# Kernel tuning notes

Hardware: AMD Instinct MI355X
Metric: run time of the kernel (lower is better)

Reference implementation:

```python
import jax, jax.numpy as jnp
import numpy as np

N_NODES = 100000
N_EDGES = 1600000
N_GRAPHS = 1024
DIM_IN = 128
DIM_SF = 32
DIM_OUT = 8
EPS = 1e-5


def setup_inputs() -> dict:
    key = jax.random.key(0)
    ks = jax.random.split(key, 16)
    feat = jax.random.normal(ks[0], (N_NODES, DIM_IN), dtype=jnp.float32)
    self_feat = jax.random.normal(ks[1], (N_GRAPHS, DIM_SF), dtype=jnp.float32)
    src = jax.random.randint(ks[2], (N_EDGES,), 0, N_NODES)
    dst = jax.random.randint(ks[3], (N_EDGES,), 0, N_NODES)
    node2graph = jnp.sort(jax.random.randint(ks[4], (N_NODES,), 0, N_GRAPHS))

    def lin(k, din, dout):
        s = 1.0 / np.sqrt(din)
        kw, kb = jax.random.split(k)
        W = jax.random.uniform(kw, (din, dout), minval=-s, maxval=s, dtype=jnp.float32)
        b = jax.random.uniform(kb, (dout,), minval=-s, maxval=s, dtype=jnp.float32)
        return W, b

    W1, b1 = lin(ks[5], DIM_IN, 100)
    W2, b2 = lin(ks[6], 100, 20)
    Wf1, bf1 = lin(ks[7], 20 * DIM_SF, 128)
    Wf2, bf2 = lin(ks[8], 128, 32)
    Wf3, bf3 = lin(ks[9], 32, DIM_OUT)
    g1 = jnp.ones((128,), jnp.float32); be1 = jnp.zeros((128,), jnp.float32)
    g2 = jnp.ones((32,), jnp.float32); be2 = jnp.zeros((32,), jnp.float32)
    return dict(feat=feat, self_feat=self_feat, src=src, dst=dst,
                node2graph=node2graph, W1=W1, b1=b1, W2=W2, b2=b2,
                Wf1=Wf1, bf1=bf1, g1=g1, be1=be1,
                Wf2=Wf2, bf2=bf2, g2=g2, be2=be2, Wf3=Wf3, bf3=bf3)


def _gcn_layer(h, src, dst, W, b):
    # copy_u + mean reduce: segment-mean of source features onto destinations.
    n = h.shape[0]
    msum = jax.ops.segment_sum(h[src], dst, num_segments=n)        # [N, d]
    deg = jax.ops.segment_sum(jnp.ones((src.shape[0], 1), h.dtype), dst,
                              num_segments=n)                      # [N, 1]
    # DGL: nodes with no incoming messages keep their previous 'h'.
    agg = jnp.where(deg > 0, msum / jnp.maximum(deg, 1.0), h)
    return agg @ W + b


def _bn(x, gamma, beta):
    # BatchNorm1d in training mode: biased batch statistics.
    mu = jnp.mean(x, axis=0)
    var = jnp.mean((x - mu) ** 2, axis=0)
    return (x - mu) / jnp.sqrt(var + EPS) * gamma + beta


def reference(feat, self_feat, src, dst, node2graph,
              W1, b1, W2, b2, Wf1, bf1, g1, be1, Wf2, bf2, g2, be2, Wf3, bf3):
    h = jax.nn.relu(_gcn_layer(feat, src, dst, W1, b1))            # [N, 100]
    h = jax.nn.relu(_gcn_layer(h, src, dst, W2, b2))               # [N, 20]
    # dgl.mean_nodes: per-graph mean pooling
    hsum = jax.ops.segment_sum(h, node2graph, num_segments=N_GRAPHS)
    cnt = jax.ops.segment_sum(jnp.ones((h.shape[0], 1), h.dtype), node2graph,
                              num_segments=N_GRAPHS)
    hg = hsum / jnp.maximum(cnt, 1.0)                              # [G, 20]
    # Kronecker fusion: bmm(hg[:, :, None], self_feat[:, None, :])
    fused = (hg[:, :, None] * self_feat[:, None, :]).reshape(hg.shape[0], -1)
    out = jax.nn.relu(_bn(fused @ Wf1 + bf1, g1, be1))
    out = jax.nn.relu(_bn(out @ Wf2 + bf2, g2, be2))
    return out @ Wf3 + bf3                                         # [G, 8]
```

## Files before the change

### kernel.cpp

```cpp
#include <hip/hip_runtime.h>
#include <hip/hip_fp16.h>

#define N_NODES 100000
#define N_EDGES 1600000
#define N_GRAPHS 1024
#define DIM_IN 128
#define D1 100
#define D1P 128
#define D2 20
#define D2P 32
#define DIM_SF 32
#define DF1 128
#define DF2 32
#define DOUT 8
#define EPS 1e-5f

typedef _Float16 hh2 __attribute__((ext_vector_type(2)));

__device__ __forceinline__ void fdacc(unsigned u, float& lo, float& hi) {
  const hh2 MLO = {(_Float16)1.0f, (_Float16)0.0f};
  const hh2 MHI = {(_Float16)0.0f, (_Float16)1.0f};
  hh2 h = __builtin_bit_cast(hh2, u);
  lo = __builtin_amdgcn_fdot2(h, MLO, lo, false);
  hi = __builtin_amdgcn_fdot2(h, MHI, hi, false);
}

__device__ __forceinline__ unsigned pkadd(unsigned a, unsigned b) {
  __half2 x = __builtin_bit_cast(__half2, a);
  __half2 y = __builtin_bit_cast(__half2, b);
  return __builtin_bit_cast(unsigned, __hadd2(x, y));
}

#define NBK 512
#define BW 196
#define EPB 4096
#define NBLK1 ((N_EDGES + EPB - 1) / EPB)

__global__ void __launch_bounds__(256) k_bcount(const int* __restrict__ dst,
                                                int* __restrict__ counts) {
  __shared__ int hist[NBK];
  int t = threadIdx.x, blk = blockIdx.x;
  for (int i = t; i < NBK; i += 256) hist[i] = 0;
  __syncthreads();
  int base = blk * EPB;
#pragma unroll
  for (int r = 0; r < 16; r++) {
    int e = base + r * 256 + t;
    if (e < N_EDGES) {
      unsigned b = (unsigned)dst[e] / BW;
      atomicAdd(&hist[b], 1);
    }
  }
  __syncthreads();
  for (int i = t; i < NBK; i += 256) counts[blk * NBK + i] = hist[i];
}

__global__ void __launch_bounds__(64) k_bscanA(const int* __restrict__ counts,
                                               int* __restrict__ offs,
                                               int* __restrict__ totals) {
  int b = blockIdx.x, l = threadIdx.x;
  int carry = 0;
  for (int chunk = 0; chunk < NBLK1; chunk += 64) {
    int blk = chunk + l;
    int v = (blk < NBLK1) ? counts[blk * NBK + b] : 0;
    int incl = v;
    for (int s = 1; s < 64; s <<= 1) { int x = __shfl_up(incl, s); if (l >= s) incl += x; }
    if (blk < NBLK1) offs[blk * NBK + b] = carry + incl - v;
    carry += __shfl(incl, 63);
  }
  if (l == 0) totals[b] = carry;
}

__global__ void __launch_bounds__(512) k_bscanB(const int* __restrict__ totals,
                                                int* __restrict__ bin_base) {
  __shared__ int lds[NBK];
  int t = threadIdx.x;
  int v = totals[t];
  lds[t] = v; __syncthreads();
  for (int s = 1; s < NBK; s <<= 1) {
    int x = (t >= s) ? lds[t - s] : 0;
    __syncthreads();
    lds[t] += x;
    __syncthreads();
  }
  bin_base[t] = lds[t] - v;
  if (t == NBK - 1) bin_base[NBK] = lds[t];
}

__global__ void __launch_bounds__(256) k_bscatter(const int* __restrict__ src,
                                                  const int* __restrict__ dst,
                                                  const int* __restrict__ offs,
                                                  const int* __restrict__ bin_base,
                                                  unsigned* __restrict__ packed_out) {
  __shared__ int hist[NBK];
  __shared__ int lbase[NBK];
  __shared__ int gbase[NBK];
  __shared__ int ssum[256];
  __shared__ unsigned sval[EPB];
  __shared__ int spos[EPB];
  int t = threadIdx.x, blk = blockIdx.x;
  for (int i = t; i < NBK; i += 256) hist[i] = 0;
  __syncthreads();
  int base = blk * EPB;
  unsigned pk[16]; int bn[16]; int rk[16];
#pragma unroll
  for (int r = 0; r < 16; r++) {
    int e = base + r * 256 + t;
    bn[r] = -1;
    if (e < N_EDGES) {
      int dv = dst[e];
      unsigned b = (unsigned)dv / BW;
      unsigned ld = (unsigned)dv - b * BW;
      bn[r] = (int)b;
      pk[r] = ((unsigned)src[e] << 8) | ld;
      rk[r] = atomicAdd(&hist[b], 1);
    }
  }
  __syncthreads();
  int h0 = hist[2 * t], h1 = hist[2 * t + 1];
  int s = h0 + h1;
  ssum[t] = s; __syncthreads();
  for (int off = 1; off < 256; off <<= 1) {
    int x = (t >= off) ? ssum[t - off] : 0;
    __syncthreads();
    ssum[t] += x;
    __syncthreads();
  }
  int excl = ssum[t] - s;
  lbase[2 * t] = excl;
  lbase[2 * t + 1] = excl + h0;
  gbase[2 * t]     = bin_base[2 * t]     + offs[blk * NBK + 2 * t];
  gbase[2 * t + 1] = bin_base[2 * t + 1] + offs[blk * NBK + 2 * t + 1];
  __syncthreads();
#pragma unroll
  for (int r = 0; r < 16; r++) {
    if (bn[r] >= 0) {
      int li = lbase[bn[r]] + rk[r];
      sval[li] = pk[r];
      spos[li] = gbase[bn[r]] + rk[r];
    }
  }
  __syncthreads();
  int cnt = N_EDGES - base; if (cnt > EPB) cnt = EPB;
  for (int i = t; i < cnt; i += 256) packed_out[spos[i]] = sval[i];
}

__global__ void __launch_bounds__(256) k_bfine(const unsigned* __restrict__ packed_in,
                                               const int* __restrict__ bin_base,
                                               int* __restrict__ csr,
                                               int* __restrict__ deg,
                                               int* __restrict__ row_off) {
  __shared__ unsigned sval[EPB];
  __shared__ int scsr[EPB];
  __shared__ int hist[256];
  __shared__ int soff[256];
  __shared__ int cur[256];
  int b = blockIdx.x, t = threadIdx.x;
  int start = bin_base[b];
  int cnt = bin_base[b + 1] - start;
  if (cnt > EPB) cnt = EPB;
  hist[t] = 0;
  __syncthreads();
  for (int i = t; i < cnt; i += 256) {
    unsigned v = packed_in[start + i];
    sval[i] = v;
    atomicAdd(&hist[v & 255u], 1);
  }
  __syncthreads();
  int h = hist[t];
  soff[t] = h; __syncthreads();
  for (int off = 1; off < 256; off <<= 1) {
    int x = (t >= off) ? soff[t - off] : 0;
    __syncthreads();
    soff[t] += x;
    __syncthreads();
  }
  int excl = soff[t] - h;
  cur[t] = excl;
  int n = b * BW + t;
  if (t < BW && n < N_NODES) { deg[n] = h; row_off[n] = start + excl; }
  __syncthreads();
  for (int i = t; i < cnt; i += 256) {
    unsigned v = sval[i];
    int pos = atomicAdd(&cur[v & 255u], 1);
    scsr[pos] = (int)(v >> 8);
  }
  __syncthreads();
  for (int i = t; i < cnt; i += 256) csr[start + i] = scsr[i];
}

__global__ void __launch_bounds__(256) k_goff(const int* __restrict__ n2g,
                                              int* __restrict__ g_off) {
  int g = blockIdx.x * 256 + threadIdx.x;
  if (g > N_GRAPHS) return;
  if (g == N_GRAPHS) { g_off[g] = N_NODES; return; }
  int lo = 0, hi = N_NODES;
  while (lo < hi) {
    int mid = (lo + hi) >> 1;
    if (n2g[mid] < g) lo = mid + 1; else hi = mid;
  }
  g_off[g] = lo;
}

__global__ void __launch_bounds__(256) k_gemm1(const float* __restrict__ feat,
                                               const float* __restrict__ W1,
                                               __half* __restrict__ p1h) {
  __shared__ float w1s[DIM_IN * D1];
  int t = threadIdx.x;
  for (int i = t; i < DIM_IN * D1; i += 256) w1s[i] = W1[i];
  __syncthreads();
  if (t >= 250) return;
  int q = t % 25, ng = t / 25;
  int n0 = blockIdx.x * 40 + ng * 4;
  int c0 = q * 4;
  float acc[4][4] = {{0.f}};
  const float* f0 = feat + (size_t)n0 * DIM_IN;
  for (int k = 0; k < DIM_IN; k += 4) {
    float4 w0 = *(const float4*)&w1s[(k + 0) * D1 + c0];
    float4 w1 = *(const float4*)&w1s[(k + 1) * D1 + c0];
    float4 w2 = *(const float4*)&w1s[(k + 2) * D1 + c0];
    float4 w3 = *(const float4*)&w1s[(k + 3) * D1 + c0];
#pragma unroll
    for (int j = 0; j < 4; j++) {
      float4 f = *(const float4*)(f0 + j * DIM_IN + k);
      acc[j][0] += f.x * w0.x + f.y * w1.x + f.z * w2.x + f.w * w3.x;
      acc[j][1] += f.x * w0.y + f.y * w1.y + f.z * w2.y + f.w * w3.y;
      acc[j][2] += f.x * w0.z + f.y * w1.z + f.z * w2.z + f.w * w3.z;
      acc[j][3] += f.x * w0.w + f.y * w1.w + f.z * w2.w + f.w * w3.w;
    }
  }
#pragma unroll
  for (int j = 0; j < 4; j++) {
    __half2* d2 = (__half2*)(p1h + (size_t)(n0 + j) * D1P + c0);
    d2[0] = __floats2half2_rn(acc[j][0], acc[j][1]);
    d2[1] = __floats2half2_rn(acc[j][2], acc[j][3]);
  }
}

__device__ __forceinline__ void acc8d(uint4 r, float4& A, float4& B) {
  fdacc(r.x, A.x, A.y);
  fdacc(r.y, A.z, A.w);
  fdacc(r.z, B.x, B.y);
  fdacc(r.w, B.z, B.w);
}

__global__ void __launch_bounds__(256) k_agg1(const __half* __restrict__ p1h,
                                              const int* __restrict__ deg,
                                              const int* __restrict__ row_off,
                                              const int* __restrict__ csr,
                                              const float* __restrict__ b1,
                                              const float* __restrict__ W2,
                                              __half* __restrict__ p2h) {
  __shared__ float w2s[D1 * D2];
  __shared__ float b1s[D1];
  __shared__ float hbuf[4][104];
  int t = threadIdx.x;
  for (int i = t; i < D1 * D2; i += 256) w2s[i] = W2[i];
  if (t < D1) b1s[t] = b1[t];
  __syncthreads();
  int w = t >> 6, lane = t & 63;
  int n = blockIdx.x * 4 + w;
  int g = lane >> 4, o = lane & 15;
  int d = deg[n], ro = row_off[n];
  float4 A = {0.f, 0.f, 0.f, 0.f}, B = {0.f, 0.f, 0.f, 0.f};
  const size_t oh = (size_t)(o * 8);
  if (d > 0) {
    for (int base = 0; base < d; base += 64) {
      int m = d - base; if (m > 64) m = 64;
      int sv = (lane < m) ? csr[ro + base + lane] : 0;
      int nr = m >> 2;
      int r = 0;
      for (; r + 1 < nr; r += 2) {
        int sA = __shfl(sv, r * 4 + g);
        int sB = __shfl(sv, r * 4 + 4 + g);
        uint4 ra = *(const uint4*)(p1h + (size_t)sA * D1P + oh);
        uint4 rb = *(const uint4*)(p1h + (size_t)sB * D1P + oh);
        uint4 rc;
        rc.x = pkadd(ra.x, rb.x); rc.y = pkadd(ra.y, rb.y);
        rc.z = pkadd(ra.z, rb.z); rc.w = pkadd(ra.w, rb.w);
        acc8d(rc, A, B);
      }
      if (r < nr) {
        int sA = __shfl(sv, r * 4 + g);
        uint4 ra = *(const uint4*)(p1h + (size_t)sA * D1P + oh);
        acc8d(ra, A, B);
      }
      int rem = m & 3;
      int sT = __shfl(sv, nr * 4 + g);
      if (rem && g < rem) {
        uint4 ra = *(const uint4*)(p1h + (size_t)sT * D1P + oh);
        acc8d(ra, A, B);
      }
    }
  } else {
    if (g == 0) {
      uint4 ra = *(const uint4*)(p1h + (size_t)n * D1P + oh);
      acc8d(ra, A, B);
    }
  }
  float v[8] = {A.x, A.y, A.z, A.w, B.x, B.y, B.z, B.w};
#pragma unroll
  for (int j = 0; j < 8; j++) {
    v[j] += __shfl_down(v[j], 32);
    v[j] += __shfl_down(v[j], 16);
  }
  if (lane < 13) {
    float inv = (d > 0) ? 1.0f / (float)d : 1.0f;
#pragma unroll
    for (int j = 0; j < 8; j++) {
      int ch = 8 * lane + j;
      if (ch < D1) hbuf[w][ch] = fmaxf(v[j] * inv + b1s[ch], 0.f);
    }
  }
  __syncthreads();
  int p = lane / 20;
  int j20 = lane - p * 20;
  int cbeg = (p == 0) ? 0 : (p == 1) ? 33 : 66;
  int cend = (p == 0) ? 33 : (p == 1) ? 66 : 100;
  if (p >= 3) { cbeg = 0; cend = 0; }
  float acc = 0.f;
  for (int c = cbeg; c < cend; c++) acc += hbuf[w][c] * w2s[c * D2 + j20];
  float t1 = __shfl_down(acc, 20);
  float t2 = __shfl_down(acc, 40);
  acc += t1 + t2;
  if (lane < D2)       p2h[(size_t)n * D2P + lane] = __float2half_rn(acc);
  else if (lane < D2P) p2h[(size_t)n * D2P + lane] = __float2half_rn(0.f);
}

__global__ void __launch_bounds__(512) k_agg2(const __half* __restrict__ p2h,
                                              const int* __restrict__ deg,
                                              const int* __restrict__ row_off,
                                              const int* __restrict__ csr,
                                              const float* __restrict__ b2,
                                              const int* __restrict__ g_off,
                                              float* __restrict__ hg) {
  __shared__ float ssum[D2];
  __shared__ float b2s[D2];
  int g = blockIdx.x, t = threadIdx.x;
  if (t < D2) { ssum[t] = 0.f; b2s[t] = b2[t]; }
  __syncthreads();
  const unsigned* pu = (const unsigned*)p2h;
  int n_lo = g_off[g], n_hi = g_off[g + 1];
  int total = (n_hi - n_lo) * 10;
  for (int idx = t; idx < total; idx += 512) {
    int n = n_lo + idx / 10;
    int c2 = idx % 10;
    int d = deg[n], ro = row_off[n];
    float lo, hi;
    if (d > 0) {
      float l0 = 0.f, h0 = 0.f, l1 = 0.f, h1 = 0.f;
      int e = 0;
      for (; e + 3 < d; e += 4) {
        unsigned u0 = pu[(size_t)csr[ro + e]     * 16 + c2];
        unsigned u1 = pu[(size_t)csr[ro + e + 1] * 16 + c2];
        unsigned u2 = pu[(size_t)csr[ro + e + 2] * 16 + c2];
        unsigned u3 = pu[(size_t)csr[ro + e + 3] * 16 + c2];
        fdacc(u0, l0, h0); fdacc(u1, l1, h1);
        fdacc(u2, l0, h0); fdacc(u3, l1, h1);
      }
      for (; e < d; e++) {
        unsigned u = pu[(size_t)csr[ro + e] * 16 + c2];
        fdacc(u, l0, h0);
      }
      float inv = 1.0f / (float)d;
      lo = (l0 + l1) * inv; hi = (h0 + h1) * inv;
    } else {
      lo = 0.f; hi = 0.f;
      fdacc(pu[(size_t)n * 16 + c2], lo, hi);
    }
    atomicAdd(&ssum[2 * c2],     fmaxf(lo + b2s[2 * c2],     0.f));
    atomicAdd(&ssum[2 * c2 + 1], fmaxf(hi + b2s[2 * c2 + 1], 0.f));
  }
  __syncthreads();
  if (t < D2) {
    int cnt = n_hi - n_lo;
    float inv = (cnt > 0) ? 1.0f / (float)cnt : 0.f;
    hg[g * D2 + t] = ssum[t] * inv;
  }
}

__global__ void __launch_bounds__(128) k_mlp1(const float* __restrict__ hg,
                                              const float* __restrict__ sf,
                                              const float* __restrict__ Wf1,
                                              const float* __restrict__ bf1,
                                              float* __restrict__ y1) {
  __shared__ float prod[D2 * DIM_SF];
  __shared__ float hgl[D2], sfl[DIM_SF];
  int g = blockIdx.x, t = threadIdx.x;
  if (t < D2) hgl[t] = hg[g * D2 + t];
  if (t < DIM_SF) sfl[t] = sf[g * DIM_SF + t];
  __syncthreads();
  for (int i = t; i < D2 * DIM_SF; i += 128) prod[i] = hgl[i >> 5] * sfl[i & 31];
  __syncthreads();
  float acc = bf1[t];
#pragma unroll 4
  for (int k = 0; k < D2 * DIM_SF; k++) acc += prod[k] * Wf1[k * DF1 + t];
  y1[g * DF1 + t] = acc;
}

__global__ void k_bnstats(const float* __restrict__ x, int ld,
                          float* __restrict__ mu, float* __restrict__ rstd) {
  __shared__ float ssum[256], ssq[256];
  int c = blockIdx.x, t = threadIdx.x;
  float s = 0.f, q = 0.f;
  for (int r = t; r < N_GRAPHS; r += 256) { float v = x[r * ld + c]; s += v; q += v * v; }
  ssum[t] = s; ssq[t] = q; __syncthreads();
  for (int off = 128; off > 0; off >>= 1) {
    if (t < off) { ssum[t] += ssum[t + off]; ssq[t] += ssq[t + off]; }
    __syncthreads();
  }
  if (t == 0) {
    float m = ssum[0] / (float)N_GRAPHS;
    float var = ssq[0] / (float)N_GRAPHS - m * m;
    mu[c] = m;
    rstd[c] = rsqrtf(var + EPS);
  }
}

__global__ void k_mlp2(const float* __restrict__ y1, const float* __restrict__ mu1,
                       const float* __restrict__ rstd1, const float* __restrict__ g1,
                       const float* __restrict__ be1, const float* __restrict__ Wf2,
                       const float* __restrict__ bf2, float* __restrict__ y2) {
  int idx = blockIdx.x * 256 + threadIdx.x;
  int g = idx >> 5, o = idx & 31;
  float acc = bf2[o];
  for (int k = 0; k < DF1; k++) {
    float x = (y1[g * DF1 + k] - mu1[k]) * rstd1[k] * g1[k] + be1[k];
    x = fmaxf(x, 0.f);
    acc += x * Wf2[k * DF2 + o];
  }
  y2[g * DF2 + o] = acc;
}

__global__ void k_mlp3(const float* __restrict__ y2, const float* __restrict__ mu2,
                       const float* __restrict__ rstd2, const float* __restrict__ g2,
                       const float* __restrict__ be2, const float* __restrict__ Wf3,
                       const float* __restrict__ bf3, float* __restrict__ out) {
  int idx = blockIdx.x * 256 + threadIdx.x;
  int g = idx >> 3, o = idx & 7;
  float acc = bf3[o];
  for (int k = 0; k < DF2; k++) {
    float x = (y2[g * DF2 + k] - mu2[k]) * rstd2[k] * g2[k] + be2[k];
    x = fmaxf(x, 0.f);
    acc += x * Wf3[k * DOUT + o];
  }
  out[g * DOUT + o] = acc;
}

extern "C" void kernel_launch(void* const* d_in, const int* in_sizes, int n_in,
                              void* d_out, int out_size, void* d_ws, size_t ws_size,
                              hipStream_t stream) {
  const float* feat = (const float*)d_in[0];
  const float* sf   = (const float*)d_in[1];
  const int*   src  = (const int*)d_in[2];
  const int*   dst  = (const int*)d_in[3];
  const int*   n2g  = (const int*)d_in[4];
  const float* W1   = (const float*)d_in[5];
  const float* b1   = (const float*)d_in[6];
  const float* W2   = (const float*)d_in[7];
  const float* b2   = (const float*)d_in[8];
  const float* Wf1  = (const float*)d_in[9];
  const float* bf1  = (const float*)d_in[10];
  const float* g1   = (const float*)d_in[11];
  const float* be1  = (const float*)d_in[12];
  const float* Wf2  = (const float*)d_in[13];
  const float* bf2  = (const float*)d_in[14];
  const float* g2   = (const float*)d_in[15];
  const float* be2  = (const float*)d_in[16];
  const float* Wf3  = (const float*)d_in[17];
  const float* bf3  = (const float*)d_in[18];
  float* out = (float*)d_out;

  char* ws = (char*)d_ws;
  size_t off = 0;
  auto alloc = [&](size_t bytes) -> void* {
    void* p = ws + off;
    off = (off + bytes + 255) & ~(size_t)255;
    return p;
  };
  int*      g_offs   = (int*)alloc((N_GRAPHS + 1) * 4);
  float*    hg       = (float*)alloc(N_GRAPHS * D2 * 4);
  int*      deg      = (int*)alloc(N_NODES * 4);
  int*      row_off  = (int*)alloc(N_NODES * 4);
  int*      counts   = (int*)alloc((size_t)NBLK1 * NBK * 4);
  int*      offs     = (int*)alloc((size_t)NBLK1 * NBK * 4);
  int*      totals   = (int*)alloc(NBK * 4);
  int*      bin_base = (int*)alloc((NBK + 1) * 4);
  unsigned* packed   = (unsigned*)alloc((size_t)N_EDGES * 4);
  int*      csr      = (int*)alloc((size_t)N_EDGES * 4);
  __half*   p1h      = (__half*)alloc((size_t)N_NODES * D1P * 2);
  __half*   p2h      = (__half*)alloc((size_t)N_NODES * D2P * 2);
  float*    y1       = (float*)alloc((size_t)N_GRAPHS * DF1 * 4);
  float*    y2       = (float*)alloc((size_t)N_GRAPHS * DF2 * 4);
  float*    mu1      = (float*)alloc(DF1 * 4);
  float*    rstd1    = (float*)alloc(DF1 * 4);
  float*    mu2      = (float*)alloc(DF2 * 4);
  float*    rstd2    = (float*)alloc(DF2 * 4);

  k_goff<<<(N_GRAPHS + 1 + 255) / 256, 256, 0, stream>>>(n2g, g_offs);
  k_bcount<<<NBLK1, 256, 0, stream>>>(dst, counts);
  k_bscanA<<<NBK, 64, 0, stream>>>(counts, offs, totals);
  k_bscanB<<<1, NBK, 0, stream>>>(totals, bin_base);
  k_bscatter<<<NBLK1, 256, 0, stream>>>(src, dst, offs, bin_base, packed);
  k_bfine<<<NBK, 256, 0, stream>>>(packed, bin_base, csr, deg, row_off);
  k_gemm1<<<N_NODES / 40, 256, 0, stream>>>(feat, W1, p1h);
  k_agg1<<<N_NODES / 4, 256, 0, stream>>>(p1h, deg, row_off, csr, b1, W2, p2h);
  k_agg2<<<N_GRAPHS, 512, 0, stream>>>(p2h, deg, row_off, csr, b2, g_offs, hg);
  k_mlp1<<<N_GRAPHS, 128, 0, stream>>>(hg, sf, Wf1, bf1, y1);
  k_bnstats<<<DF1, 256, 0, stream>>>(y1, DF1, mu1, rstd1);
  k_mlp2<<<(N_GRAPHS * DF2) / 256, 256, 0, stream>>>(y1, mu1, rstd1, g1, be1, Wf2, bf2, y2);
  k_bnstats<<<DF2, 256, 0, stream>>>(y2, DF2, mu2, rstd2);
  k_mlp3<<<(N_GRAPHS * DOUT) / 256, 256, 0, stream>>>(y2, mu2, rstd2, g2, be2, Wf3, bf3, out);
}
```

Baseline: 400.9 us.

## Replace bucket count/scan with atomic fixed-stride buckets and retile GCN kernels

Drops the count and two scan kernels of the edge bucket sort. Buckets now reserve slots with global atomics into fixed EPB-sized regions, and the bucket counters are zeroed by a memset. k_gemm1 computes 8 nodes per thread instead of 4, and k_agg1 handles 8 nodes per wave with a 4-way unrolled gather. k_agg2 reads 4 channels per thread with uint2 loads. This cuts launches and global scan traffic. The risks are that bucket order inside a bin becomes nondeterministic and that any bin with more than EPB edges would overflow.

```diff
diff --git a/kernel.cpp b/kernel.cpp
--- a/kernel.cpp
+++ b/kernel.cpp
@@ -14,6 +14,7 @@
 #define DF2 32
 #define DOUT 8
 #define EPS 1e-5f
+#define NPW 8
 
 typedef _Float16 hh2 __attribute__((ext_vector_type(2)));
 
@@ -36,61 +37,9 @@
 #define EPB 4096
 #define NBLK1 ((N_EDGES + EPB - 1) / EPB)
 
-__global__ void __launch_bounds__(256) k_bcount(const int* __restrict__ dst,
-                                                int* __restrict__ counts) {
-  __shared__ int hist[NBK];
-  int t = threadIdx.x, blk = blockIdx.x;
-  for (int i = t; i < NBK; i += 256) hist[i] = 0;
-  __syncthreads();
-  int base = blk * EPB;
-#pragma unroll
-  for (int r = 0; r < 16; r++) {
-    int e = base + r * 256 + t;
-    if (e < N_EDGES) {
-      unsigned b = (unsigned)dst[e] / BW;
-      atomicAdd(&hist[b], 1);
-    }
-  }
-  __syncthreads();
-  for (int i = t; i < NBK; i += 256) counts[blk * NBK + i] = hist[i];
-}
-
-__global__ void __launch_bounds__(64) k_bscanA(const int* __restrict__ counts,
-                                               int* __restrict__ offs,
-                                               int* __restrict__ totals) {
-  int b = blockIdx.x, l = threadIdx.x;
-  int carry = 0;
-  for (int chunk = 0; chunk < NBLK1; chunk += 64) {
-    int blk = chunk + l;
-    int v = (blk < NBLK1) ? counts[blk * NBK + b] : 0;
-    int incl = v;
-    for (int s = 1; s < 64; s <<= 1) { int x = __shfl_up(incl, s); if (l >= s) incl += x; }
-    if (blk < NBLK1) offs[blk * NBK + b] = carry + incl - v;
-    carry += __shfl(incl, 63);
-  }
-  if (l == 0) totals[b] = carry;
-}
-
-__global__ void __launch_bounds__(512) k_bscanB(const int* __restrict__ totals,
-                                                int* __restrict__ bin_base) {
-  __shared__ int lds[NBK];
-  int t = threadIdx.x;
-  int v = totals[t];
-  lds[t] = v; __syncthreads();
-  for (int s = 1; s < NBK; s <<= 1) {
-    int x = (t >= s) ? lds[t - s] : 0;
-    __syncthreads();
-    lds[t] += x;
-    __syncthreads();
-  }
-  bin_base[t] = lds[t] - v;
-  if (t == NBK - 1) bin_base[NBK] = lds[t];
-}
-
 __global__ void __launch_bounds__(256) k_bscatter(const int* __restrict__ src,
                                                   const int* __restrict__ dst,
-                                                  const int* __restrict__ offs,
-                                                  const int* __restrict__ bin_base,
+                                                  int* __restrict__ bucket_cnt,
                                                   unsigned* __restrict__ packed_out) {
   __shared__ int hist[NBK];
   __shared__ int lbase[NBK];
@@ -129,8 +78,8 @@
   int excl = ssum[t] - s;
   lbase[2 * t] = excl;
   lbase[2 * t + 1] = excl + h0;
-  gbase[2 * t]     = bin_base[2 * t]     + offs[blk * NBK + 2 * t];
-  gbase[2 * t + 1] = bin_base[2 * t + 1] + offs[blk * NBK + 2 * t + 1];
+  gbase[2 * t]     = (h0 > 0) ? (2 * t) * EPB     + atomicAdd(&bucket_cnt[2 * t],     h0) : 0;
+  gbase[2 * t + 1] = (h1 > 0) ? (2 * t + 1) * EPB + atomicAdd(&bucket_cnt[2 * t + 1], h1) : 0;
   __syncthreads();
 #pragma unroll
   for (int r = 0; r < 16; r++) {
@@ -146,7 +95,7 @@
 }
 
 __global__ void __launch_bounds__(256) k_bfine(const unsigned* __restrict__ packed_in,
-                                               const int* __restrict__ bin_base,
+                                               const int* __restrict__ bucket_cnt,
                                                int* __restrict__ csr,
                                                int* __restrict__ deg,
                                                int* __restrict__ row_off) {
@@ -156,8 +105,8 @@
   __shared__ int soff[256];
   __shared__ int cur[256];
   int b = blockIdx.x, t = threadIdx.x;
-  int start = bin_base[b];
-  int cnt = bin_base[b + 1] - start;
+  int start = b * EPB;
+  int cnt = bucket_cnt[b];
   if (cnt > EPB) cnt = EPB;
   hist[t] = 0;
   __syncthreads();
@@ -211,9 +160,9 @@
   __syncthreads();
   if (t >= 250) return;
   int q = t % 25, ng = t / 25;
-  int n0 = blockIdx.x * 40 + ng * 4;
+  int n0 = blockIdx.x * 80 + ng * 8;
   int c0 = q * 4;
-  float acc[4][4] = {{0.f}};
+  float acc[8][4] = {{0.f}};
   const float* f0 = feat + (size_t)n0 * DIM_IN;
   for (int k = 0; k < DIM_IN; k += 4) {
     float4 w0 = *(const float4*)&w1s[(k + 0) * D1 + c0];
@@ -221,7 +170,7 @@
     float4 w2 = *(const float4*)&w1s[(k + 2) * D1 + c0];
     float4 w3 = *(const float4*)&w1s[(k + 3) * D1 + c0];
 #pragma unroll
-    for (int j = 0; j < 4; j++) {
+    for (int j = 0; j < 8; j++) {
       float4 f = *(const float4*)(f0 + j * DIM_IN + k);
       acc[j][0] += f.x * w0.x + f.y * w1.x + f.z * w2.x + f.w * w3.x;
       acc[j][1] += f.x * w0.y + f.y * w1.y + f.z * w2.y + f.w * w3.y;
@@ -230,7 +179,7 @@
     }
   }
 #pragma unroll
-  for (int j = 0; j < 4; j++) {
+  for (int j = 0; j < 8; j++) {
     __half2* d2 = (__half2*)(p1h + (size_t)(n0 + j) * D1P + c0);
     d2[0] = __floats2half2_rn(acc[j][0], acc[j][1]);
     d2[1] = __floats2half2_rn(acc[j][2], acc[j][3]);
@@ -259,72 +208,92 @@
   if (t < D1) b1s[t] = b1[t];
   __syncthreads();
   int w = t >> 6, lane = t & 63;
-  int n = blockIdx.x * 4 + w;
   int g = lane >> 4, o = lane & 15;
-  int d = deg[n], ro = row_off[n];
-  float4 A = {0.f, 0.f, 0.f, 0.f}, B = {0.f, 0.f, 0.f, 0.f};
   const size_t oh = (size_t)(o * 8);
-  if (d > 0) {
-    for (int base = 0; base < d; base += 64) {
-      int m = d - base; if (m > 64) m = 64;
-      int sv = (lane < m) ? csr[ro + base + lane] : 0;
-      int nr = m >> 2;
-      int r = 0;
-      for (; r + 1 < nr; r += 2) {
-        int sA = __shfl(sv, r * 4 + g);
-        int sB = __shfl(sv, r * 4 + 4 + g);
-        uint4 ra = *(const uint4*)(p1h + (size_t)sA * D1P + oh);
-        uint4 rb = *(const uint4*)(p1h + (size_t)sB * D1P + oh);
-        uint4 rc;
-        rc.x = pkadd(ra.x, rb.x); rc.y = pkadd(ra.y, rb.y);
-        rc.z = pkadd(ra.z, rb.z); rc.w = pkadd(ra.w, rb.w);
-        acc8d(rc, A, B);
-      }
-      if (r < nr) {
-        int sA = __shfl(sv, r * 4 + g);
-        uint4 ra = *(const uint4*)(p1h + (size_t)sA * D1P + oh);
-        acc8d(ra, A, B);
-      }
-      int rem = m & 3;
-      int sT = __shfl(sv, nr * 4 + g);
-      if (rem && g < rem) {
-        uint4 ra = *(const uint4*)(p1h + (size_t)sT * D1P + oh);
-        acc8d(ra, A, B);
-      }
-    }
-  } else {
-    if (g == 0) {
-      uint4 ra = *(const uint4*)(p1h + (size_t)n * D1P + oh);
-      acc8d(ra, A, B);
-    }
-  }
-  float v[8] = {A.x, A.y, A.z, A.w, B.x, B.y, B.z, B.w};
-#pragma unroll
-  for (int j = 0; j < 8; j++) {
-    v[j] += __shfl_down(v[j], 32);
-    v[j] += __shfl_down(v[j], 16);
-  }
-  if (lane < 13) {
-    float inv = (d > 0) ? 1.0f / (float)d : 1.0f;
-#pragma unroll
-    for (int j = 0; j < 8; j++) {
-      int ch = 8 * lane + j;
-      if (ch < D1) hbuf[w][ch] = fmaxf(v[j] * inv + b1s[ch], 0.f);
-    }
-  }
-  __syncthreads();
   int p = lane / 20;
   int j20 = lane - p * 20;
   int cbeg = (p == 0) ? 0 : (p == 1) ? 33 : 66;
   int cend = (p == 0) ? 33 : (p == 1) ? 66 : 100;
   if (p >= 3) { cbeg = 0; cend = 0; }
-  float acc = 0.f;
-  for (int c = cbeg; c < cend; c++) acc += hbuf[w][c] * w2s[c * D2 + j20];
-  float t1 = __shfl_down(acc, 20);
-  float t2 = __shfl_down(acc, 40);
-  acc += t1 + t2;
-  if (lane < D2)       p2h[(size_t)n * D2P + lane] = __float2half_rn(acc);
-  else if (lane < D2P) p2h[(size_t)n * D2P + lane] = __float2half_rn(0.f);
+  int n0 = (blockIdx.x * 4 + w) * NPW;
+  for (int nn = 0; nn < NPW; nn++) {
+    int n = n0 + nn;
+    int d = deg[n], ro = row_off[n];
+    float4 A = {0.f, 0.f, 0.f, 0.f}, B = {0.f, 0.f, 0.f, 0.f};
+    if (d > 0) {
+      for (int base = 0; base < d; base += 64) {
+        int m = d - base; if (m > 64) m = 64;
+        int sv = (lane < m) ? csr[ro + base + lane] : 0;
+        int nr = m >> 2;
+        int r = 0;
+        for (; r + 3 < nr; r += 4) {
+          int sA = __shfl(sv, r * 4 + g);
+          int sB = __shfl(sv, r * 4 + 4 + g);
+          int sC = __shfl(sv, r * 4 + 8 + g);
+          int sD = __shfl(sv, r * 4 + 12 + g);
+          uint4 ra = *(const uint4*)(p1h + (size_t)sA * D1P + oh);
+          uint4 rb = *(const uint4*)(p1h + (size_t)sB * D1P + oh);
+          uint4 rc = *(const uint4*)(p1h + (size_t)sC * D1P + oh);
+          uint4 rd = *(const uint4*)(p1h + (size_t)sD * D1P + oh);
+          uint4 u, v2;
+          u.x = pkadd(ra.x, rb.x); u.y = pkadd(ra.y, rb.y);
+          u.z = pkadd(ra.z, rb.z); u.w = pkadd(ra.w, rb.w);
+          v2.x = pkadd(rc.x, rd.x); v2.y = pkadd(rc.y, rd.y);
+          v2.z = pkadd(rc.z, rd.z); v2.w = pkadd(rc.w, rd.w);
+          acc8d(u, A, B);
+          acc8d(v2, A, B);
+        }
+        if (r + 1 < nr) {
+          int sA = __shfl(sv, r * 4 + g);
+          int sB = __shfl(sv, r * 4 + 4 + g);
+          uint4 ra = *(const uint4*)(p1h + (size_t)sA * D1P + oh);
+          uint4 rb = *(const uint4*)(p1h + (size_t)sB * D1P + oh);
+          uint4 u;
+          u.x = pkadd(ra.x, rb.x); u.y = pkadd(ra.y, rb.y);
+          u.z = pkadd(ra.z, rb.z); u.w = pkadd(ra.w, rb.w);
+          acc8d(u, A, B);
+          r += 2;
+        }
+        if (r < nr) {
+          int sA = __shfl(sv, r * 4 + g);
+          uint4 ra = *(const uint4*)(p1h + (size_t)sA * D1P + oh);
+          acc8d(ra, A, B);
+        }
+        int rem = m & 3;
+        int sT = __shfl(sv, nr * 4 + g);
+        if (rem && g < rem) {
+          uint4 ra = *(const uint4*)(p1h + (size_t)sT * D1P + oh);
+          acc8d(ra, A, B);
+        }
+      }
+    } else {
+      if (g == 0) {
+        uint4 ra = *(const uint4*)(p1h + (size_t)n * D1P + oh);
+        acc8d(ra, A, B);
+      }
+    }
+    float v[8] = {A.x, A.y, A.z, A.w, B.x, B.y, B.z, B.w};
+#pragma unroll
+    for (int j = 0; j < 8; j++) {
+      v[j] += __shfl_down(v[j], 32);
+      v[j] += __shfl_down(v[j], 16);
+    }
+    if (lane < 13) {
+      float inv = (d > 0) ? 1.0f / (float)d : 1.0f;
+#pragma unroll
+      for (int j = 0; j < 8; j++) {
+        int ch = 8 * lane + j;
+        if (ch < D1) hbuf[w][ch] = fmaxf(v[j] * inv + b1s[ch], 0.f);
+      }
+    }
+    float acc = 0.f;
+    for (int c = cbeg; c < cend; c++) acc += hbuf[w][c] * w2s[c * D2 + j20];
+    float t1 = __shfl_down(acc, 20);
+    float t2 = __shfl_down(acc, 40);
+    acc += t1 + t2;
+    if (lane < D2)       p2h[(size_t)n * D2P + lane] = __float2half_rn(acc);
+    else if (lane < D2P) p2h[(size_t)n * D2P + lane] = __float2half_rn(0.f);
+  }
 }
 
 __global__ void __launch_bounds__(512) k_agg2(const __half* __restrict__ p2h,
@@ -341,40 +310,52 @@
   __syncthreads();
   const unsigned* pu = (const unsigned*)p2h;
   int n_lo = g_off[g], n_hi = g_off[g + 1];
-  int total = (n_hi - n_lo) * 10;
-  for (int idx = t; idx < total; idx += 512) {
-    int n = n_lo + idx / 10;
-    int c2 = idx % 10;
-    int d = deg[n], ro = row_off[n];
-    float lo, hi;
-    if (d > 0) {
-      float l0 = 0.f, h0 = 0.f, l1 = 0.f, h1 = 0.f;
-      int e = 0;
-      for (; e + 3 < d; e += 4) {
-        unsigned u0 = pu[(size_t)csr[ro + e]     * 16 + c2];
-        unsigned u1 = pu[(size_t)csr[ro + e + 1] * 16 + c2];
-        unsigned u2 = pu[(size_t)csr[ro + e + 2] * 16 + c2];
-        unsigned u3 = pu[(size_t)csr[ro + e + 3] * 16 + c2];
-        fdacc(u0, l0, h0); fdacc(u1, l1, h1);
-        fdacc(u2, l0, h0); fdacc(u3, l1, h1);
+  int nn = n_hi - n_lo;
+  if (t < 510) {
+    int nid = t / 5, c2 = t - (t / 5) * 5;
+    int ch = 4 * c2;
+    for (int ni = nid; ni < nn; ni += 102) {
+      int n = n_lo + ni;
+      int d = deg[n], ro = row_off[n];
+      float v0, v1, v2, v3;
+      if (d > 0) {
+        float a0 = 0.f, a1 = 0.f, a2 = 0.f, a3 = 0.f;
+        float b0 = 0.f, b1 = 0.f, bb2 = 0.f, b3 = 0.f;
+        int e = 0;
+        for (; e + 3 < d; e += 4) {
+          int s0 = csr[ro + e],     s1 = csr[ro + e + 1];
+          int s2 = csr[ro + e + 2], s3 = csr[ro + e + 3];
+          uint2 r0 = *(const uint2*)(pu + (size_t)s0 * 16 + 2 * c2);
+          uint2 r1 = *(const uint2*)(pu + (size_t)s1 * 16 + 2 * c2);
+          uint2 r2 = *(const uint2*)(pu + (size_t)s2 * 16 + 2 * c2);
+          uint2 r3 = *(const uint2*)(pu + (size_t)s3 * 16 + 2 * c2);
+          fdacc(r0.x, a0, a1); fdacc(r0.y, a2, a3);
+          fdacc(r1.x, b0, b1); fdacc(r1.y, bb2, b3);
+          fdacc(r2.x, a0, a1); fdacc(r2.y, a2, a3);
+          fdacc(r3.x, b0, b1); fdacc(r3.y, bb2, b3);
+        }
+        for (; e < d; e++) {
+          int s0 = csr[ro + e];
+          uint2 r0 = *(const uint2*)(pu + (size_t)s0 * 16 + 2 * c2);
+          fdacc(r0.x, a0, a1); fdacc(r0.y, a2, a3);
+        }
+        float inv = 1.0f / (float)d;
+        v0 = (a0 + b0) * inv; v1 = (a1 + b1) * inv;
+        v2 = (a2 + bb2) * inv; v3 = (a3 + b3) * inv;
+      } else {
+        uint2 r0 = *(const uint2*)(pu + (size_t)n * 16 + 2 * c2);
+        v0 = v1 = v2 = v3 = 0.f;
+        fdacc(r0.x, v0, v1); fdacc(r0.y, v2, v3);
       }
-      for (; e < d; e++) {
-        unsigned u = pu[(size_t)csr[ro + e] * 16 + c2];
-        fdacc(u, l0, h0);
-      }
-      float inv = 1.0f / (float)d;
-      lo = (l0 + l1) * inv; hi = (h0 + h1) * inv;
-    } else {
-      lo = 0.f; hi = 0.f;
-      fdacc(pu[(size_t)n * 16 + c2], lo, hi);
-    }
-    atomicAdd(&ssum[2 * c2],     fmaxf(lo + b2s[2 * c2],     0.f));
-    atomicAdd(&ssum[2 * c2 + 1], fmaxf(hi + b2s[2 * c2 + 1], 0.f));
+      atomicAdd(&ssum[ch + 0], fmaxf(v0 + b2s[ch + 0], 0.f));
+      atomicAdd(&ssum[ch + 1], fmaxf(v1 + b2s[ch + 1], 0.f));
+      atomicAdd(&ssum[ch + 2], fmaxf(v2 + b2s[ch + 2], 0.f));
+      atomicAdd(&ssum[ch + 3], fmaxf(v3 + b2s[ch + 3], 0.f));
+    }
   }
   __syncthreads();
   if (t < D2) {
-    int cnt = n_hi - n_lo;
-    float inv = (cnt > 0) ? 1.0f / (float)cnt : 0.f;
+    float inv = (nn > 0) ? 1.0f / (float)nn : 0.f;
     hg[g * D2 + t] = ssum[t] * inv;
   }
 }
@@ -478,16 +459,14 @@
     off = (off + bytes + 255) & ~(size_t)255;
     return p;
   };
+  int*      bucket_cnt = (int*)alloc(NBK * 4);
+  size_t zero_bytes = off;
   int*      g_offs   = (int*)alloc((N_GRAPHS + 1) * 4);
   float*    hg       = (float*)alloc(N_GRAPHS * D2 * 4);
   int*      deg      = (int*)alloc(N_NODES * 4);
   int*      row_off  = (int*)alloc(N_NODES * 4);
-  int*      counts   = (int*)alloc((size_t)NBLK1 * NBK * 4);
-  int*      offs     = (int*)alloc((size_t)NBLK1 * NBK * 4);
-  int*      totals   = (int*)alloc(NBK * 4);
-  int*      bin_base = (int*)alloc((NBK + 1) * 4);
-  unsigned* packed   = (unsigned*)alloc((size_t)N_EDGES * 4);
-  int*      csr      = (int*)alloc((size_t)N_EDGES * 4);
+  unsigned* packed   = (unsigned*)alloc((size_t)NBK * EPB * 4);
+  int*      csr      = (int*)alloc((size_t)NBK * EPB * 4);
   __half*   p1h      = (__half*)alloc((size_t)N_NODES * D1P * 2);
   __half*   p2h      = (__half*)alloc((size_t)N_NODES * D2P * 2);
   float*    y1       = (float*)alloc((size_t)N_GRAPHS * DF1 * 4);
@@ -497,14 +476,13 @@
   float*    mu2      = (float*)alloc(DF2 * 4);
   float*    rstd2    = (float*)alloc(DF2 * 4);
 
+  hipMemsetAsync(d_ws, 0, zero_bytes, stream);
+
   k_goff<<<(N_GRAPHS + 1 + 255) / 256, 256, 0, stream>>>(n2g, g_offs);
-  k_bcount<<<NBLK1, 256, 0, stream>>>(dst, counts);
-  k_bscanA<<<NBK, 64, 0, stream>>>(counts, offs, totals);
-  k_bscanB<<<1, NBK, 0, stream>>>(totals, bin_base);
-  k_bscatter<<<NBLK1, 256, 0, stream>>>(src, dst, offs, bin_base, packed);
-  k_bfine<<<NBK, 256, 0, stream>>>(packed, bin_base, csr, deg, row_off);
-  k_gemm1<<<N_NODES / 40, 256, 0, stream>>>(feat, W1, p1h);
-  k_agg1<<<N_NODES / 4, 256, 0, stream>>>(p1h, deg, row_off, csr, b1, W2, p2h);
+  k_bscatter<<<NBLK1, 256, 0, stream>>>(src, dst, bucket_cnt, packed);
+  k_bfine<<<NBK, 256, 0, stream>>>(packed, bucket_cnt, csr, deg, row_off);
+  k_gemm1<<<N_NODES / 80, 256, 0, stream>>>(feat, W1, p1h);
+  k_agg1<<<N_NODES / (4 * NPW), 256, 0, stream>>>(p1h, deg, row_off, csr, b1, W2, p2h);
   k_agg2<<<N_GRAPHS, 512, 0, stream>>>(p2h, deg, row_off, csr, b2, g_offs, hg);
   k_mlp1<<<N_GRAPHS, 128, 0, stream>>>(hg, sf, Wf1, bf1, y1);
   k_bnstats<<<DF1, 256, 0, stream>>>(y1, DF1, mu1, rstd1);
```

Result: slower. 410.9 us (+2.5%).
